# Kernel tuning notes

Measured on AMD Instinct MI355X. Metric: run time of the kernel, lower is better.

Reference implementation:

```python
import jax, jax.numpy as jnp
import numpy as np

HEADS = 16
D_MODEL = 1024
MAX_LEN = 1024
BATCH = 4
SEQ = 1024


def _skew(QEr):
    # Transformer-XL / Music-Transformer skew trick.
    # QEr: [B, H, L, L] -> pad one zero column on the left, reshape, drop first row.
    B, H, L, _ = QEr.shape
    padded = jnp.pad(QEr, ((0, 0), (0, 0), (0, 0), (1, 0)))  # [B,H,L,L+1]
    reshaped = padded.reshape(B, H, L + 1, L)
    return reshaped[:, :, 1:, :]  # [B,H,L,L]


def setup_inputs() -> dict:
    key = jax.random.key(0)
    ks = jax.random.split(key, 8)
    d = D_MODEL // HEADS
    std = 0.05  # tf.random_normal_initializer default stddev
    return {
        "query": jax.random.normal(ks[0], (BATCH, SEQ, D_MODEL), jnp.float32),
        "key": jax.random.normal(ks[1], (BATCH, SEQ, D_MODEL), jnp.float32),
        "value": jax.random.normal(ks[2], (BATCH, SEQ, D_MODEL), jnp.float32),
        "WQ": std * jax.random.normal(ks[3], (D_MODEL, D_MODEL), jnp.float32),
        "WK": std * jax.random.normal(ks[4], (D_MODEL, D_MODEL), jnp.float32),
        "WV": std * jax.random.normal(ks[5], (D_MODEL, D_MODEL), jnp.float32),
        "Er": std * jax.random.normal(ks[6], (MAX_LEN, d), jnp.float32),
        "WMerge": std * jax.random.normal(ks[7], (D_MODEL, D_MODEL), jnp.float32),
    }


def reference(query, key, value, WQ, WK, WV, Er, WMerge):
    B, L, D = query.shape
    H = HEADS
    d = D // H
    # Faithful to source: plain reshape (NOT transpose-based head split).
    q = (query @ WQ).reshape(B, H, L, d)          # [B,H,L,d]
    k_t = (key @ WK).reshape(B, H, d, L)          # [B,H,d,L]
    v = (value @ WV).reshape(B, H, L, d)          # [B,H,L,d]
    start = MAX_LEN - L
    Er_t = Er[start:, :].T                        # [d, L]
    QEr = q @ Er_t                                # [B,H,L,L]
    Srel = _skew(QEr)                             # [B,H,L,L]
    attn = (q @ k_t + Srel) / jnp.sqrt(jnp.asarray(d, q.dtype))
    attn = jax.nn.softmax(attn, axis=-1)
    out = attn @ v                                # [B,H,L,d]
    out = out.transpose(0, 2, 1, 3).reshape(B, L, D)
    return out @ WMerge
```

## Files before the change

kernel.cpp:

```cpp
#include <hip/hip_runtime.h>

#define H_  16
#define L_  1024
#define D_  1024
#define DH  64

typedef short bf16x8 __attribute__((ext_vector_type(8)));
typedef float f32x4  __attribute__((ext_vector_type(4)));

__device__ __forceinline__ ushort f2bf(float f) {
  union { float f; unsigned int u; } x; x.f = f;
  unsigned int u = x.u;
  u = (u + 0x7fffu + ((u >> 16) & 1u)) >> 16;
  return (ushort)u;
}
__device__ __forceinline__ float bf2f(ushort s) {
  union { unsigned int u; float f; } x; x.u = ((unsigned int)s) << 16;
  return x.f;
}

__global__ __launch_bounds__(256) void cvt3_kernel(
    const float* __restrict__ q, const float* __restrict__ k, const float* __restrict__ v,
    ushort* __restrict__ qb, ushort* __restrict__ kb, ushort* __restrict__ vb) {
  const int z = blockIdx.y;
  const float* in = (z == 0) ? q : (z == 1) ? k : v;
  ushort* out = (z == 0) ? qb : (z == 1) ? kb : vb;
  int i = (blockIdx.x * 256 + threadIdx.x) * 8;
  float4 f0 = *(const float4*)(in + i);
  float4 f1 = *(const float4*)(in + i + 4);
  ushort u[8] = {f2bf(f0.x), f2bf(f0.y), f2bf(f0.z), f2bf(f0.w),
                 f2bf(f1.x), f2bf(f1.y), f2bf(f1.z), f2bf(f1.w)};
  *(uint4*)(out + i) = *(uint4*)u;
}

__global__ __launch_bounds__(256) void erF_kernel(const float* __restrict__ Er,
                                                  ushort* __restrict__ ErF) {
  int t = blockIdx.x * 256 + threadIdx.x;
  int lane = t & 63, ph = (t >> 6) & 1, jg = t >> 7;
  int m = jg * 16 + (lane & 15);
  int k = ph * 32 + (lane >> 4) * 8;
  float4 f0 = *(const float4*)(Er + m * 64 + k);
  float4 f1 = *(const float4*)(Er + m * 64 + k + 4);
  ushort4 u0, u1;
  u0.x = f2bf(f0.x); u0.y = f2bf(f0.y); u0.z = f2bf(f0.z); u0.w = f2bf(f0.w);
  u1.x = f2bf(f1.x); u1.y = f2bf(f1.y); u1.z = f2bf(f1.z); u1.w = f2bf(f1.w);
  *(ushort4*)(ErF + t * 8)     = u0;
  *(ushort4*)(ErF + t * 8 + 4) = u1;
}

__global__ __launch_bounds__(256) void wT4_kernel(
    const float* __restrict__ W0, const float* __restrict__ W1,
    const float* __restrict__ W2, const float* __restrict__ W3,
    ushort* __restrict__ T0, ushort* __restrict__ T1,
    ushort* __restrict__ T2, ushort* __restrict__ T3) {
  __shared__ ushort tt[64][72];
  const int z = blockIdx.z;
  const float* W = (z == 0) ? W0 : (z == 1) ? W1 : (z == 2) ? W2 : W3;
  ushort*     WT = (z == 0) ? T0 : (z == 1) ? T1 : (z == 2) ? T2 : T3;
  const int t = threadIdx.x;
  const int k0 = blockIdx.y * 64, n0 = blockIdx.x * 64;
#pragma unroll
  for (int c = 0; c < 4; ++c) {
    int k = c * 16 + (t >> 4);
    float4 f = *(const float4*)(W + (size_t)(k0 + k) * 1024 + n0 + (t & 15) * 4);
    tt[(t & 15) * 4 + 0][k] = f2bf(f.x);
    tt[(t & 15) * 4 + 1][k] = f2bf(f.y);
    tt[(t & 15) * 4 + 2][k] = f2bf(f.z);
    tt[(t & 15) * 4 + 3][k] = f2bf(f.w);
  }
  __syncthreads();
#pragma unroll
  for (int p = 0; p < 2; ++p) {
    int n = p * 32 + (t >> 3);
    *(uint4*)(WT + (size_t)(n0 + n) * 1024 + k0 + (t & 7) * 8) = *(const uint4*)(&tt[n][(t & 7) * 8]);
  }
}

__global__ __launch_bounds__(256) void gemm_qkv_kernel(
    const ushort* __restrict__ Aq, const ushort* __restrict__ Ak, const ushort* __restrict__ Av,
    const ushort* __restrict__ BTq, const ushort* __restrict__ BTk, const ushort* __restrict__ BTv,
    ushort* __restrict__ Cq, ushort* __restrict__ Ck, ushort* __restrict__ Cv) {
  __shared__ ushort lsA[128][40];
  __shared__ ushort lsB[128][40];
  const int z = blockIdx.z;
  const ushort* A  = (z == 0) ? Aq  : (z == 1) ? Ak  : Av;
  const ushort* BT = (z == 0) ? BTq : (z == 1) ? BTk : BTv;
  ushort*       Cp = (z == 0) ? Cq  : (z == 1) ? Ck  : Cv;

  const int tid  = threadIdx.x;
  const int w    = tid >> 6, lane = tid & 63, qd = lane >> 4, ln = lane & 15;
  const int rw   = w >> 1, cw = w & 1;
  const int m0   = blockIdx.y * 128, n0 = blockIdx.x * 128;

  f32x4 acc[16];
#pragma unroll
  for (int i = 0; i < 16; ++i) acc[i] = (f32x4){0.f, 0.f, 0.f, 0.f};

  for (int kb = 0; kb < 32; ++kb) {
    const int k0 = kb * 32;
    const int row = tid >> 1, half = tid & 1;
#pragma unroll
    for (int c = 0; c < 2; ++c)
      *(uint4*)(&lsA[row][half * 16 + c * 8]) =
          *(const uint4*)(A + (size_t)(m0 + row) * 1024 + k0 + half * 16 + c * 8);
#pragma unroll
    for (int c = 0; c < 2; ++c)
      *(uint4*)(&lsB[row][half * 16 + c * 8]) =
          *(const uint4*)(BT + (size_t)(n0 + row) * 1024 + k0 + half * 16 + c * 8);
    __syncthreads();
    bf16x8 afr[4], bfr[4];
#pragma unroll
    for (int am = 0; am < 4; ++am)
      afr[am] = *(const bf16x8*)(&lsA[rw * 64 + am * 16 + ln][qd * 8]);
#pragma unroll
    for (int bn = 0; bn < 4; ++bn)
      bfr[bn] = *(const bf16x8*)(&lsB[cw * 64 + bn * 16 + ln][qd * 8]);
#pragma unroll
    for (int am = 0; am < 4; ++am)
#pragma unroll
      for (int bn = 0; bn < 4; ++bn)
        acc[am * 4 + bn] = __builtin_amdgcn_mfma_f32_16x16x32_bf16(afr[am], bfr[bn], acc[am * 4 + bn], 0, 0, 0);
    __syncthreads();
  }
#pragma unroll
  for (int am = 0; am < 4; ++am)
#pragma unroll
    for (int bn = 0; bn < 4; ++bn) {
      const int rbase = m0 + rw * 64 + am * 16 + qd * 4;
      const int colg  = n0 + cw * 64 + bn * 16 + ln;
      if (z == 0) {
#pragma unroll
        for (int r = 0; r < 4; ++r)
          Cp[(size_t)(rbase + r) * 1024 + colg] = f2bf(acc[am * 4 + bn][r]);
      } else if (z == 1) {
        const int bh  = rbase >> 6;
        const int ki0 = rbase & 63;
        const int jg  = colg >> 4;
        const int ph  = ki0 >> 5;
        const int lanep = ((ki0 >> 3) & 3) * 16 + (colg & 15);
        const int jj0 = ki0 & 7;
        ushort4 u;
        u.x = f2bf(acc[am * 4 + bn][0]); u.y = f2bf(acc[am * 4 + bn][1]);
        u.z = f2bf(acc[am * 4 + bn][2]); u.w = f2bf(acc[am * 4 + bn][3]);
        *(ushort4*)(Cp + (size_t)bh * 65536 + (size_t)((jg * 2 + ph) * 64 + lanep) * 8 + jj0) = u;
      } else {
        const int bh = rbase >> 6;
        const int llow = colg >> 6, dd = colg & 63;
        const int g = dd >> 4, lnf = dd & 15;
#pragma unroll
        for (int r = 0; r < 4; ++r) {
          int l = ((rbase + r) & 63) * 16 + llow;
          int ks = l >> 5;
          int lanep = ((l >> 3) & 3) * 16 + lnf;
          int jj = l & 7;
          Cp[(size_t)bh * 65536 + (size_t)((g * 32 + ks) * 64 + lanep) * 8 + jj] = f2bf(acc[am * 4 + bn][r]);
        }
      }
    }
}

__global__ __launch_bounds__(512) void gemm_mg_kernel(const ushort* __restrict__ A,
                                                      const ushort* __restrict__ BT,
                                                      float* __restrict__ Cp) {
  __shared__ ushort ls[2][2][128][40];
  const int tid  = threadIdx.x;
  const int w    = tid >> 6, lane = tid & 63, qd = lane >> 4, ln = lane & 15;
  const int kh   = w >> 2, q = w & 3;
  const int rw   = q >> 1, cw = q & 1;
  const int m0   = blockIdx.y * 128, n0 = blockIdx.x * 128;
  const int ts   = tid >> 8, tt = tid & 255;
  const int trow = tt >> 1, thalf = tt & 1;

  f32x4 acc[16];
#pragma unroll
  for (int i = 0; i < 16; ++i) acc[i] = (f32x4){0.f, 0.f, 0.f, 0.f};

  for (int kb = 0; kb < 16; ++kb) {
    const int k0 = ts * 512 + kb * 32;
#pragma unroll
    for (int c = 0; c < 2; ++c)
      *(uint4*)(&ls[ts][0][trow][thalf * 16 + c * 8]) =
          *(const uint4*)(A + (size_t)(m0 + trow) * 1024 + k0 + thalf * 16 + c * 8);
#pragma unroll
    for (int c = 0; c < 2; ++c)
      *(uint4*)(&ls[ts][1][trow][thalf * 16 + c * 8]) =
          *(const uint4*)(BT + (size_t)(n0 + trow) * 1024 + k0 + thalf * 16 + c * 8);
    __syncthreads();
    bf16x8 afr[4], bfr[4];
#pragma unroll
    for (int am = 0; am < 4; ++am)
      afr[am] = *(const bf16x8*)(&ls[kh][0][rw * 64 + am * 16 + ln][qd * 8]);
#pragma unroll
    for (int bn = 0; bn < 4; ++bn)
      bfr[bn] = *(const bf16x8*)(&ls[kh][1][cw * 64 + bn * 16 + ln][qd * 8]);
#pragma unroll
    for (int am = 0; am < 4; ++am)
#pragma unroll
      for (int bn = 0; bn < 4; ++bn)
        acc[am * 4 + bn] = __builtin_amdgcn_mfma_f32_16x16x32_bf16(afr[am], bfr[bn], acc[am * 4 + bn], 0, 0, 0);
    __syncthreads();
  }

  float* red = (float*)&ls[0][0][0][0];
  for (int half = 0; half < 2; ++half) {
    __syncthreads();
    if (w >= 4) {
      const int base = ((w - 4) * 64 + lane) * 33;
#pragma unroll
      for (int i = 0; i < 8; ++i)
#pragma unroll
        for (int c = 0; c < 4; ++c) red[base + i * 4 + c] = acc[half * 8 + i][c];
    }
    __syncthreads();
    if (w < 4) {
      const int base = (w * 64 + lane) * 33;
#pragma unroll
      for (int i = 0; i < 8; ++i)
#pragma unroll
        for (int c = 0; c < 4; ++c) acc[half * 8 + i][c] += red[base + i * 4 + c];
    }
  }
  if (w < 4) {
#pragma unroll
    for (int am = 0; am < 4; ++am)
#pragma unroll
      for (int bn = 0; bn < 4; ++bn) {
        const int rbase = m0 + rw * 64 + am * 16 + qd * 4;
        const int colg  = n0 + cw * 64 + bn * 16 + ln;
#pragma unroll
        for (int r = 0; r < 4; ++r)
          Cp[(size_t)(rbase + r) * 1024 + colg] = acc[am * 4 + bn][r];
      }
  }
}

__global__ __launch_bounds__(512, 4) void attn_kernel(
    const ushort* __restrict__ QW, const ushort* __restrict__ KF,
    const ushort* __restrict__ VF, const ushort* __restrict__ ErF,
    ushort* __restrict__ Om) {
  __shared__ ushort qflat[17440];
  __shared__ float  red[4][64][4];
  __shared__ float  stats[2][8][16];

  const int tid  = threadIdx.x;
  const int w    = tid >> 6;
  const int lane = tid & 63;
  const int qd   = lane >> 4;
  const int ln   = lane & 15;
  const int bh   = blockIdx.y;
  const int i0   = blockIdx.x << 4;
  const ushort* q  = QW + ((size_t)bh << 16);
  const ushort* kf = KF + ((size_t)bh << 16);
  const ushort* vf = VF + ((size_t)bh << 16);

  if (tid < 16) qflat[tid * 1025 + 1024] = 0;

  bf16x8 a00 = *(const bf16x8*)(q + (size_t)(i0 + ln) * 64 + qd * 8);
  bf16x8 a01 = *(const bf16x8*)(q + (size_t)(i0 + ln) * 64 + 32 + qd * 8);
  const int row16 = (i0 + 16 > 1023) ? 1023 : i0 + 16;
  bf16x8 a10 = *(const bf16x8*)(q + (size_t)row16 * 64 + qd * 8);
  bf16x8 a11 = *(const bf16x8*)(q + (size_t)row16 * 64 + 32 + qd * 8);

  const int jg0 = w * 8;

#pragma unroll
  for (int f = 0; f < 8; ++f) {
    const int jg = jg0 + f;
    bf16x8 b0 = *(const bf16x8*)(ErF + (size_t)((jg * 2 + 0) * 64 + lane) * 8);
    bf16x8 b1 = *(const bf16x8*)(ErF + (size_t)((jg * 2 + 1) * 64 + lane) * 8);
    f32x4 acc = {0.f, 0.f, 0.f, 0.f};
    acc = __builtin_amdgcn_mfma_f32_16x16x32_bf16(a00, b0, acc, 0, 0, 0);
    acc = __builtin_amdgcn_mfma_f32_16x16x32_bf16(a01, b1, acc, 0, 0, 0);
    const int m = jg * 16 + ln;
#pragma unroll
    for (int r = 0; r < 4; ++r) qflat[(qd * 4 + r) * 1025 + m] = f2bf(acc[r]);
    if (jg * 16 <= 1006 - i0) {
      f32x4 ac2 = {0.f, 0.f, 0.f, 0.f};
      ac2 = __builtin_amdgcn_mfma_f32_16x16x32_bf16(a10, b0, ac2, 0, 0, 0);
      ac2 = __builtin_amdgcn_mfma_f32_16x16x32_bf16(a11, b1, ac2, 0, 0, 0);
      if (qd == 0) qflat[16 * 1025 + m] = f2bf(ac2[0]);
    }
  }

  f32x4 sfr[8];
#pragma unroll
  for (int f = 0; f < 8; ++f) {
    const int jg = jg0 + f;
    bf16x8 b0 = *(const bf16x8*)(kf + (size_t)((jg * 2 + 0) * 64 + lane) * 8);
    bf16x8 b1 = *(const bf16x8*)(kf + (size_t)((jg * 2 + 1) * 64 + lane) * 8);
    f32x4 acc = {0.f, 0.f, 0.f, 0.f};
    acc = __builtin_amdgcn_mfma_f32_16x16x32_bf16(a00, b0, acc, 0, 0, 0);
    acc = __builtin_amdgcn_mfma_f32_16x16x32_bf16(a01, b1, acc, 0, 0, 0);
    sfr[f] = acc;
  }
  __syncthreads();

#pragma unroll
  for (int f = 0; f < 8; ++f) {
    const int cj = 1023 - i0 + w * 128 + f * 16 + ln;
#pragma unroll
    for (int r = 0; r < 4; ++r)
      sfr[f][r] += bf2f(qflat[(qd * 4 + r) * 1024 + cj]);
  }

  {
    float vm[4];
#pragma unroll
    for (int r = 0; r < 4; ++r) {
      float m = sfr[0][r];
#pragma unroll
      for (int f = 1; f < 8; ++f) m = fmaxf(m, sfr[f][r]);
#pragma unroll
      for (int off = 1; off < 16; off <<= 1) m = fmaxf(m, __shfl_xor(m, off, 64));
      vm[r] = m;
    }
    if (ln == 0) {
#pragma unroll
      for (int r = 0; r < 4; ++r) stats[0][w][qd * 4 + r] = vm[r];
    }
  }
  __syncthreads();
  const float cexp = 0.18033688011112042f;
  float gm2[4];
#pragma unroll
  for (int r = 0; r < 4; ++r) {
    float m = stats[0][0][qd * 4 + r];
#pragma unroll
    for (int ww = 1; ww < 8; ++ww) m = fmaxf(m, stats[0][ww][qd * 4 + r]);
    gm2[r] = -m * cexp;
  }

  float vs[4] = {0.f, 0.f, 0.f, 0.f};
#pragma unroll
  for (int f = 0; f < 8; ++f) {
    const int j = w * 128 + f * 16 + ln;
#pragma unroll
    for (int r = 0; r < 4; ++r) {
      float e = exp2f(fmaf(sfr[f][r], cexp, gm2[r]));
      vs[r] += e;
      qflat[(qd * 4 + r) * 1048 + j] = f2bf(e);
    }
  }
#pragma unroll
  for (int r = 0; r < 4; ++r) {
    float s = vs[r];
#pragma unroll
    for (int off = 1; off < 16; off <<= 1) s += __shfl_xor(s, off, 64);
    if (ln == 0) stats[1][w][qd * 4 + r] = s;
  }
  __syncthreads();
  float rrl[4];
#pragma unroll
  for (int r = 0; r < 4; ++r) {
    float s = 0.f;
#pragma unroll
    for (int ww = 0; ww < 8; ++ww) s += stats[1][ww][qd * 4 + r];
    rrl[r] = 1.0f / s;
  }

  const int g = w & 3, kh = w >> 2;
  f32x4 oacc = {0.f, 0.f, 0.f, 0.f};
#pragma unroll
  for (int kc = 0; kc < 16; ++kc) {
    const int ks = kh * 16 + kc;
    bf16x8 ap = *(const bf16x8*)(qflat + ln * 1048 + ks * 32 + qd * 8);
    bf16x8 bv = *(const bf16x8*)(vf + (size_t)((g * 32 + ks) * 64 + lane) * 8);
    oacc = __builtin_amdgcn_mfma_f32_16x16x32_bf16(ap, bv, oacc, 0, 0, 0);
  }

  if (w >= 4) {
#pragma unroll
    for (int cc = 0; cc < 4; ++cc) red[w - 4][lane][cc] = oacc[cc];
  }
  __syncthreads();
  if (w < 4) {
    const int b = bh >> 4, h = bh & 15;
    ushort* ob = Om + ((size_t)b * L_ * D_) + (size_t)h * DH + (size_t)(g * 16 + ln);
#pragma unroll
    for (int r = 0; r < 4; ++r) {
      float o = oacc[r] + red[w][lane][r];
      int row = i0 + qd * 4 + r;
      ob[(size_t)row * D_] = f2bf(o * rrl[r]);
    }
  }
}

extern "C" void kernel_launch(void* const* d_in, const int* in_sizes, int n_in,
                              void* d_out, int out_size, void* d_ws, size_t ws_size,
                              hipStream_t stream) {
  const float* query = (const float*)d_in[0];
  const float* key   = (const float*)d_in[1];
  const float* value = (const float*)d_in[2];
  const float* WQ    = (const float*)d_in[3];
  const float* WK    = (const float*)d_in[4];
  const float* WV    = (const float*)d_in[5];
  const float* Er    = (const float*)d_in[6];
  const float* WM    = (const float*)d_in[7];
  float* out = (float*)d_out;

  ushort* QW  = (ushort*)d_ws;
  ushort* KF  = QW  + (size_t)4096 * 1024;
  ushort* VF  = KF  + (size_t)4096 * 1024;
  ushort* O   = VF  + (size_t)4096 * 1024;
  ushort* ErF = O   + (size_t)4096 * 1024;
  ushort* WTQ = ErF + (size_t)65536;
  ushort* WTK = WTQ + (size_t)1024 * 1024;
  ushort* WTV = WTK + (size_t)1024 * 1024;
  ushort* WTM = WTV + (size_t)1024 * 1024;
  ushort* KB  = WTM + (size_t)1024 * 1024;
  ushort* VB  = KB  + (size_t)4096 * 1024;
  ushort* QB  = O;

  cvt3_kernel<<<dim3(2048, 3), 256, 0, stream>>>(query, key, value, QB, KB, VB);
  wT4_kernel<<<dim3(16, 16, 4), 256, 0, stream>>>(WQ, WK, WV, WM, WTQ, WTK, WTV, WTM);
  erF_kernel<<<32, 256, 0, stream>>>(Er, ErF);

  gemm_qkv_kernel<<<dim3(8, 32, 3), 256, 0, stream>>>(QB, KB, VB,
                                                      WTQ, WTK, WTV,
                                                      QW, KF, VF);

  attn_kernel<<<dim3(64, 64), 512, 0, stream>>>(QW, KF, VF, ErF, O);

  gemm_mg_kernel<<<dim3(8, 32), 512, 0, stream>>>(O, WTM, out);
}
```

Baseline: 298.0 us.

## Pre-tile GEMM operands into MFMA fragment layout and load via global_load_lds

Producer kernels (input conversion, weight transpose, attention output) now write bf16 operands in a blocked layout that matches the 16x16x32 MFMA fragment order. Each 128x32 tile becomes contiguous, so both GEMM kernels can copy it straight into LDS with global_load_lds 16-byte transfers instead of staging through registers with padded rows. This cuts VGPR staging and address math and gives contiguous global reads. The cost is scattered stores in the producers, and unpadded LDS reads that may cause bank conflicts.

```diff
diff --git a/kernel.cpp b/kernel.cpp
--- a/kernel.cpp
+++ b/kernel.cpp
@@ -17,6 +17,17 @@
 __device__ __forceinline__ float bf2f(ushort s) {
   union { unsigned int u; float f; } x; x.u = ((unsigned int)s) << 16;
   return x.f;
+}
+
+__device__ __forceinline__ size_t afi(int m, int k) {
+  return (((size_t)((m >> 7) * 32 + (k >> 5)) * 8 + ((m >> 4) & 7)) << 9)
+       + ((size_t)((((k >> 3) & 3) << 4) + (m & 15)) << 3) + (k & 7);
+}
+
+__device__ __forceinline__ void gl_lds16(const ushort* g, ushort* l) {
+  __builtin_amdgcn_global_load_lds(
+      (const __attribute__((address_space(1))) void*)g,
+      (__attribute__((address_space(3))) void*)l, 16, 0, 0);
 }
 
 __global__ __launch_bounds__(256) void cvt3_kernel(
@@ -25,12 +36,13 @@
   const int z = blockIdx.y;
   const float* in = (z == 0) ? q : (z == 1) ? k : v;
   ushort* out = (z == 0) ? qb : (z == 1) ? kb : vb;
-  int i = (blockIdx.x * 256 + threadIdx.x) * 8;
-  float4 f0 = *(const float4*)(in + i);
-  float4 f1 = *(const float4*)(in + i + 4);
+  int idx = (blockIdx.x * 256 + threadIdx.x) * 8;
+  int m = idx >> 10, kk = idx & 1023;
+  float4 f0 = *(const float4*)(in + idx);
+  float4 f1 = *(const float4*)(in + idx + 4);
   ushort u[8] = {f2bf(f0.x), f2bf(f0.y), f2bf(f0.z), f2bf(f0.w),
                  f2bf(f1.x), f2bf(f1.y), f2bf(f1.z), f2bf(f1.w)};
-  *(uint4*)(out + i) = *(uint4*)u;
+  *(uint4*)(out + afi(m, kk)) = *(uint4*)u;
 }
 
 __global__ __launch_bounds__(256) void erF_kernel(const float* __restrict__ Er,
@@ -72,7 +84,7 @@
 #pragma unroll
   for (int p = 0; p < 2; ++p) {
     int n = p * 32 + (t >> 3);
-    *(uint4*)(WT + (size_t)(n0 + n) * 1024 + k0 + (t & 7) * 8) = *(const uint4*)(&tt[n][(t & 7) * 8]);
+    *(uint4*)(WT + afi(n0 + n, k0 + (t & 7) * 8)) = *(const uint4*)(&tt[n][(t & 7) * 8]);
   }
 }
 
@@ -80,8 +92,8 @@
     const ushort* __restrict__ Aq, const ushort* __restrict__ Ak, const ushort* __restrict__ Av,
     const ushort* __restrict__ BTq, const ushort* __restrict__ BTk, const ushort* __restrict__ BTv,
     ushort* __restrict__ Cq, ushort* __restrict__ Ck, ushort* __restrict__ Cv) {
-  __shared__ ushort lsA[128][40];
-  __shared__ ushort lsB[128][40];
+  __shared__ ushort lsA[4096];
+  __shared__ ushort lsB[4096];
   const int z = blockIdx.z;
   const ushort* A  = (z == 0) ? Aq  : (z == 1) ? Ak  : Av;
   const ushort* BT = (z == 0) ? BTq : (z == 1) ? BTk : BTv;
@@ -90,31 +102,29 @@
   const int tid  = threadIdx.x;
   const int w    = tid >> 6, lane = tid & 63, qd = lane >> 4, ln = lane & 15;
   const int rw   = w >> 1, cw = w & 1;
-  const int m0   = blockIdx.y * 128, n0 = blockIdx.x * 128;
+  const int mb   = blockIdx.y, nb = blockIdx.x;
+  const int m0   = mb * 128, n0 = nb * 128;
 
   f32x4 acc[16];
 #pragma unroll
   for (int i = 0; i < 16; ++i) acc[i] = (f32x4){0.f, 0.f, 0.f, 0.f};
 
   for (int kb = 0; kb < 32; ++kb) {
-    const int k0 = kb * 32;
-    const int row = tid >> 1, half = tid & 1;
-#pragma unroll
-    for (int c = 0; c < 2; ++c)
-      *(uint4*)(&lsA[row][half * 16 + c * 8]) =
-          *(const uint4*)(A + (size_t)(m0 + row) * 1024 + k0 + half * 16 + c * 8);
-#pragma unroll
-    for (int c = 0; c < 2; ++c)
-      *(uint4*)(&lsB[row][half * 16 + c * 8]) =
-          *(const uint4*)(BT + (size_t)(n0 + row) * 1024 + k0 + half * 16 + c * 8);
+    const ushort* Ab = A  + ((size_t)(mb * 32 + kb) << 12);
+    const ushort* Bb = BT + ((size_t)(nb * 32 + kb) << 12);
+    const int c0 = 2 * w;
+    gl_lds16(Ab + ((size_t)c0 << 9) + lane * 8,        lsA + (c0 << 9));
+    gl_lds16(Ab + ((size_t)(c0 + 1) << 9) + lane * 8,  lsA + ((c0 + 1) << 9));
+    gl_lds16(Bb + ((size_t)c0 << 9) + lane * 8,        lsB + (c0 << 9));
+    gl_lds16(Bb + ((size_t)(c0 + 1) << 9) + lane * 8,  lsB + ((c0 + 1) << 9));
     __syncthreads();
     bf16x8 afr[4], bfr[4];
 #pragma unroll
     for (int am = 0; am < 4; ++am)
-      afr[am] = *(const bf16x8*)(&lsA[rw * 64 + am * 16 + ln][qd * 8]);
+      afr[am] = *(const bf16x8*)(lsA + ((rw * 4 + am) << 9) + lane * 8);
 #pragma unroll
     for (int bn = 0; bn < 4; ++bn)
-      bfr[bn] = *(const bf16x8*)(&lsB[cw * 64 + bn * 16 + ln][qd * 8]);
+      bfr[bn] = *(const bf16x8*)(lsB + ((cw * 4 + bn) << 9) + lane * 8);
 #pragma unroll
     for (int am = 0; am < 4; ++am)
 #pragma unroll
@@ -162,37 +172,37 @@
 __global__ __launch_bounds__(512) void gemm_mg_kernel(const ushort* __restrict__ A,
                                                       const ushort* __restrict__ BT,
                                                       float* __restrict__ Cp) {
-  __shared__ ushort ls[2][2][128][40];
+  __shared__ ushort lsA[2][4096];
+  __shared__ ushort lsB[2][4096];
+  __shared__ float  mgred[256 * 33];
   const int tid  = threadIdx.x;
   const int w    = tid >> 6, lane = tid & 63, qd = lane >> 4, ln = lane & 15;
   const int kh   = w >> 2, q = w & 3;
   const int rw   = q >> 1, cw = q & 1;
-  const int m0   = blockIdx.y * 128, n0 = blockIdx.x * 128;
-  const int ts   = tid >> 8, tt = tid & 255;
-  const int trow = tt >> 1, thalf = tt & 1;
+  const int mb   = blockIdx.y, nb = blockIdx.x;
+  const int m0   = mb * 128, n0 = nb * 128;
 
   f32x4 acc[16];
 #pragma unroll
   for (int i = 0; i < 16; ++i) acc[i] = (f32x4){0.f, 0.f, 0.f, 0.f};
 
   for (int kb = 0; kb < 16; ++kb) {
-    const int k0 = ts * 512 + kb * 32;
-#pragma unroll
-    for (int c = 0; c < 2; ++c)
-      *(uint4*)(&ls[ts][0][trow][thalf * 16 + c * 8]) =
-          *(const uint4*)(A + (size_t)(m0 + trow) * 1024 + k0 + thalf * 16 + c * 8);
-#pragma unroll
-    for (int c = 0; c < 2; ++c)
-      *(uint4*)(&ls[ts][1][trow][thalf * 16 + c * 8]) =
-          *(const uint4*)(BT + (size_t)(n0 + trow) * 1024 + k0 + thalf * 16 + c * 8);
+    const int kbi = kh * 16 + kb;
+    const ushort* Ab = A  + ((size_t)(mb * 32 + kbi) << 12);
+    const ushort* Bb = BT + ((size_t)(nb * 32 + kbi) << 12);
+    const int c0 = 2 * q;
+    gl_lds16(Ab + ((size_t)c0 << 9) + lane * 8,        lsA[kh] + (c0 << 9));
+    gl_lds16(Ab + ((size_t)(c0 + 1) << 9) + lane * 8,  lsA[kh] + ((c0 + 1) << 9));
+    gl_lds16(Bb + ((size_t)c0 << 9) + lane * 8,        lsB[kh] + (c0 << 9));
+    gl_lds16(Bb + ((size_t)(c0 + 1) << 9) + lane * 8,  lsB[kh] + ((c0 + 1) << 9));
     __syncthreads();
     bf16x8 afr[4], bfr[4];
 #pragma unroll
     for (int am = 0; am < 4; ++am)
-      afr[am] = *(const bf16x8*)(&ls[kh][0][rw * 64 + am * 16 + ln][qd * 8]);
+      afr[am] = *(const bf16x8*)(lsA[kh] + ((rw * 4 + am) << 9) + lane * 8);
 #pragma unroll
     for (int bn = 0; bn < 4; ++bn)
-      bfr[bn] = *(const bf16x8*)(&ls[kh][1][cw * 64 + bn * 16 + ln][qd * 8]);
+      bfr[bn] = *(const bf16x8*)(lsB[kh] + ((cw * 4 + bn) << 9) + lane * 8);
 #pragma unroll
     for (int am = 0; am < 4; ++am)
 #pragma unroll
@@ -201,7 +211,6 @@
     __syncthreads();
   }
 
-  float* red = (float*)&ls[0][0][0][0];
   for (int half = 0; half < 2; ++half) {
     __syncthreads();
     if (w >= 4) {
@@ -209,7 +218,7 @@
 #pragma unroll
       for (int i = 0; i < 8; ++i)
 #pragma unroll
-        for (int c = 0; c < 4; ++c) red[base + i * 4 + c] = acc[half * 8 + i][c];
+        for (int c = 0; c < 4; ++c) mgred[base + i * 4 + c] = acc[half * 8 + i][c];
     }
     __syncthreads();
     if (w < 4) {
@@ -217,7 +226,7 @@
 #pragma unroll
       for (int i = 0; i < 8; ++i)
 #pragma unroll
-        for (int c = 0; c < 4; ++c) acc[half * 8 + i][c] += red[base + i * 4 + c];
+        for (int c = 0; c < 4; ++c) acc[half * 8 + i][c] += mgred[base + i * 4 + c];
     }
   }
   if (w < 4) {
@@ -375,12 +384,14 @@
   __syncthreads();
   if (w < 4) {
     const int b = bh >> 4, h = bh & 15;
-    ushort* ob = Om + ((size_t)b * L_ * D_) + (size_t)h * DH + (size_t)(g * 16 + ln);
+    const int kg = h * 64 + g * 16 + ln;
+    const int mbase = b * 1024 + i0;
+    ushort* ob = Om + (((size_t)((mbase >> 7) * 32 + (kg >> 5)) * 8 + ((mbase >> 4) & 7)) << 9)
+               + ((((kg >> 3) & 3) * 16 + qd * 4) << 3) + (kg & 7);
 #pragma unroll
     for (int r = 0; r < 4; ++r) {
       float o = oacc[r] + red[w][lane][r];
-      int row = i0 + qd * 4 + r;
-      ob[(size_t)row * D_] = f2bf(o * rrl[r]);
+      ob[r * 8] = f2bf(o * rrl[r]);
     }
   }
 }
```

New measurement: 277.1 us. 7.0% less time.
